# Performance work log

Hardware: AMD Instinct MI355X
Metric: run time of the kernel (lower is better)

Reference implementation:

```python
import jax, jax.numpy as jnp
import numpy as np

B, M, EMB, K = 32768, 2048, 128, 8
TAU = 0.3

def setup_inputs() -> dict:
    key = jax.random.key(0)
    ks = jax.random.split(key, 6)
    return {
        "Gl_cur": jax.random.normal(ks[0], (B, 2), dtype=jnp.float32),
        "ancL": jax.random.normal(ks[1], (B, M, 2), dtype=jnp.float32),
        "W1": jax.random.normal(ks[2], (EMB, 2), dtype=jnp.float32) * 0.5,
        "b1": jax.random.normal(ks[3], (EMB,), dtype=jnp.float32) * 0.1,
        "W2": jax.random.normal(ks[4], (EMB, EMB), dtype=jnp.float32) * (1.0 / np.sqrt(EMB)),
        "b2": jax.random.normal(ks[5], (EMB,), dtype=jnp.float32) * 0.1,
    }

def reference(Gl_cur, ancL, W1, b1, W2, b2):
    # pairwise squared distances: [B, M]
    d2 = jnp.sum((ancL - Gl_cur[:, None, :]) ** 2, axis=-1)
    # top-k nearest anchors (topk of -d2, as in torch code)
    vals, idxs = jax.lax.top_k(-d2, K)              # vals: [B,K] (negated d2)
    topA = jnp.take_along_axis(ancL, idxs[:, :, None], axis=1)  # [B,K,2]
    # 2-layer GELU MLP (exact/erf GELU, torch default); dropout inactive in eval
    h1 = jax.nn.gelu(jnp.einsum('bkc,ec->bke', topA, W1) + b1, approximate=False)
    topE = jax.nn.gelu(jnp.einsum('bke,fe->bkf', h1, W2) + b2, approximate=False)
    # softmax combine: w = softmax(vals / -tau) = softmax(d2_top / tau), faithful to source
    w = jax.nn.softmax(vals / (-TAU), axis=1)       # [B,K]
    return jnp.sum(topE * w[:, :, None], axis=1)    # [B, EMB]
```

## Files before the change

### kernel.cpp

```cpp
#include <hip/hip_runtime.h>
#include <hip/hip_bf16.h>
#include <math.h>

#define NB   32768
#define NM   2048
#define NEMB 128
#define NK   8
#define TAU  0.3f
#define FLT_BIG 3.402823466e38f

typedef __attribute__((ext_vector_type(8))) short bf16x8;
typedef __attribute__((ext_vector_type(4))) float f32x4;

__device__ __forceinline__ float gelu_tanh(float x) {
    const float x2 = x * x;
    const float u  = fmaf(0.044715f, x2, 1.0f);
    const float a  = x * u * (-2.3022082f);
    const float e  = __builtin_amdgcn_exp2f(a);
    const float r  = __builtin_amdgcn_rcpf(e + 1.0f);
    return x * r;
}
__device__ __forceinline__ unsigned pack2(float lo, float hi) {
    __hip_bfloat162 b = __float22bfloat162_rn(make_float2(lo, hi));
    return *reinterpret_cast<unsigned*>(&b);
}

template<int CTRL>
__device__ __forceinline__ unsigned dpp_umin(unsigned v) {
    const unsigned t = (unsigned)__builtin_amdgcn_update_dpp(0, (int)v, CTRL, 0xF, 0xF, true);
    return v < t ? v : t;
}
template<int CTRL>
__device__ __forceinline__ float dpp_fadd(float v) {
    const float t = __int_as_float(__builtin_amdgcn_update_dpp(0, __float_as_int(v), CTRL, 0xF, 0xF, true));
    return v + t;
}

template<int DEPTH>
__device__ __forceinline__ int extract8(float (&ld)[DEPTH], unsigned (&lp)[DEPTH],
                                        float (&td)[8], unsigned (&tp)[8], const int lane) {
    int pops = 0;
#pragma unroll
    for (int k = 0; k < 8; ++k) {
        const unsigned key = __float_as_uint(ld[0]);
        unsigned m = key;
        m = dpp_umin<0xB1>(m);  m = dpp_umin<0x4E>(m);
        m = dpp_umin<0x141>(m); m = dpp_umin<0x140>(m);
        { unsigned t = __shfl_xor(m, 16); m = m < t ? m : t;
          t = __shfl_xor(m, 32);          m = m < t ? m : t; }
        const unsigned long long mk = __ballot(key == m);
        const int src = __ffsll(mk) - 1;
        td[k] = __uint_as_float(m);
        tp[k] = __shfl(lp[0], src);
        if (lane == src) {
#pragma unroll
            for (int j = 0; j < DEPTH - 1; ++j) { ld[j] = ld[j + 1]; lp[j] = lp[j + 1]; }
            ld[DEPTH - 1] = FLT_BIG;
            ++pops;
        }
    }
    return pops;
}

__global__ void __launch_bounds__(512, 6) fused_anchor_mlp(
    const float* __restrict__ Gl, const float* __restrict__ ancL,
    const float* __restrict__ W1, const float* __restrict__ b1,
    const float* __restrict__ W2, const float* __restrict__ b2,
    float* __restrict__ out)
{
    __shared__ uint4  w2s[2048];
    __shared__ uint4  h1s4[1024];
    __shared__ float4 b2s4[32];
    __shared__ float  wts[8][8];

    const int tid  = threadIdx.x;
    const int wave = tid >> 6;
    const int lane = tid & 63;
    const int pair = wave >> 1;
    const int half = wave & 1;
    const int rowbase = blockIdx.x << 3;
    const int row  = rowbase + wave;

    {
        const float4* w2f = reinterpret_cast<const float4*>(W2);
        for (int i = tid; i < 2048; i += 512) {
            const float4 lo = w2f[i * 2], hi = w2f[i * 2 + 1];
            uint4 u;
            u.x = pack2(lo.x, lo.y); u.y = pack2(lo.z, lo.w);
            u.z = pack2(hi.x, hi.y); u.w = pack2(hi.z, hi.w);
            w2s[(i & ~15) | ((i & 15) ^ ((i >> 4) & 7))] = u;
        }
        if (tid < 32) b2s4[tid] = reinterpret_cast<const float4*>(b2)[tid];
    }

    const float2 g = reinterpret_cast<const float2*>(Gl)[row];
    const f32x4* a4 = reinterpret_cast<const f32x4*>(ancL) + (size_t)row * (NM / 2);

    float    bd[3];
    unsigned bp[3];
#pragma unroll
    for (int i = 0; i < 3; ++i) { bd[i] = FLT_BIG; bp[i] = 0u; }

    auto ins3 = [&](float d, unsigned p) {
        const bool c0 = d < bd[0], c1 = d < bd[1], c2 = d < bd[2];
        const float n2 = __builtin_amdgcn_fmed3f(d, bd[1], bd[2]);
        const float n1 = __builtin_amdgcn_fmed3f(d, bd[0], bd[1]);
        const float n0 = fminf(d, bd[0]);
        bp[2] = c1 ? bp[1] : (c2 ? p : bp[2]);
        bp[1] = c0 ? bp[0] : (c1 ? p : bp[1]);
        bp[0] = c0 ? p : bp[0];
        bd[2] = n2; bd[1] = n1; bd[0] = n0;
    };

    f32x4 buf[3];
#pragma unroll
    for (int j = 0; j < 3; ++j) buf[j] = __builtin_nontemporal_load(&a4[j * 64 + lane]);

#pragma unroll
    for (int it = 0; it < 16; ++it) {
        const int slot = it % 3;
        const f32x4 v = buf[slot];
        if (it + 3 < 16)
            buf[slot] = __builtin_nontemporal_load(&a4[(it + 3) * 64 + lane]);
        const float dx0 = v.x - g.x, dy0 = v.y - g.y;
        const float dx1 = v.z - g.x, dy1 = v.w - g.y;
        const float d0 = __fadd_rn(__fmul_rn(dx0, dx0), __fmul_rn(dy0, dy0));
        const float d1 = __fadd_rn(__fmul_rn(dx1, dx1), __fmul_rn(dy1, dy1));
        ins3(d0, pack2(v.x, v.y));
        ins3(d1, pack2(v.z, v.w));
    }

    float    td[8];
    unsigned tp[8];
    const int pops = extract8<3>(bd, bp, td, tp, lane);

    if (__ballot(pops == 3)) {
        float    fd[8];
        unsigned fp[8];
#pragma unroll
        for (int i = 0; i < 8; ++i) { fd[i] = FLT_BIG; fp[i] = 0u; }
        for (int it = 0; it < 16; ++it) {
            const f32x4 vv = a4[it * 64 + lane];
#pragma unroll
            for (int h = 0; h < 2; ++h) {
                const float ax = h ? vv.z : vv.x;
                const float ay = h ? vv.w : vv.y;
                const float ddx = ax - g.x, ddy = ay - g.y;
                const float d = __fadd_rn(__fmul_rn(ddx, ddx), __fmul_rn(ddy, ddy));
                if (d < fd[7]) {
                    const unsigned p = pack2(ax, ay);
#pragma unroll
                    for (int j = 7; j >= 1; --j) {
                        const bool s1 = fd[j - 1] > d;
                        const bool s2 = fd[j] > d;
                        const float    nd = s1 ? fd[j - 1] : (s2 ? d : fd[j]);
                        const unsigned np = s1 ? fp[j - 1] : (s2 ? p : fp[j]);
                        fd[j] = nd; fp[j] = np;
                    }
                    if (fd[0] > d) { fd[0] = d; fp[0] = p; }
                }
            }
        }
        (void)extract8<8>(fd, fp, td, tp, lane);
    }

    const float mx = td[7];
    float ek[8], ssum = 0.f;
#pragma unroll
    for (int k = 0; k < 8; ++k) { ek[k] = __expf((td[k] - mx) * (1.0f / TAU)); ssum += ek[k]; }
    const float inv = 1.0f / ssum;
    float wv = 0.f;
#pragma unroll
    for (int k = 0; k < 8; ++k) wv = (lane == k) ? ek[k] * inv : wv;
    if (lane < 8) wts[wave][lane] = wv;

    const float4 w1v = reinterpret_cast<const float4*>(W1)[lane];
    const float2 b1v = reinterpret_cast<const float2*>(b1)[lane];
    unsigned* h1w = reinterpret_cast<unsigned*>(h1s4 + (pair << 8));
#pragma unroll
    for (int k = 0; k < 8; ++k) {
        const unsigned pk = tp[k];
        const float ax = __uint_as_float(pk << 16);
        const float ay = __uint_as_float(pk & 0xFFFF0000u);
        const float x0 = fmaf(ax, w1v.x, fmaf(ay, w1v.y, b1v.x));
        const float x1 = fmaf(ax, w1v.z, fmaf(ay, w1v.w, b1v.y));
        const int r = (half << 3) + k;
        h1w[(r << 6) + ((((lane >> 2) ^ k) << 2) | (lane & 3))] = pack2(gelu_tanh(x0), gelu_tanh(x1));
    }
    __syncthreads();

    const uint4* h1b = h1s4 + (pair << 8);
    const int bslot = lane >> 4, bxor = lane & 7, brow = (lane & 15) * 16;
    bf16x8 bq0 = __builtin_bit_cast(bf16x8, h1b[brow + (( 0 + bslot) ^ bxor)]);
    bf16x8 bq1 = __builtin_bit_cast(bf16x8, h1b[brow + (( 4 + bslot) ^ bxor)]);
    bf16x8 bq2 = __builtin_bit_cast(bf16x8, h1b[brow + (( 8 + bslot) ^ bxor)]);
    bf16x8 bq3 = __builtin_bit_cast(bf16x8, h1b[brow + ((12 + bslot) ^ bxor)]);

    const float wsel = wts[(pair << 1) | ((lane >> 3) & 1)][lane & 7];

#pragma unroll 2
    for (int i = 0; i < 4; ++i) {
        const int ft = (half << 2) + i;
        const int arow = (ft * 16 + (lane & 15)) * 16;
        f32x4 acc = {0.f, 0.f, 0.f, 0.f};
        acc = __builtin_amdgcn_mfma_f32_16x16x32_bf16(
                  __builtin_bit_cast(bf16x8, w2s[arow + (( 0 + bslot) ^ bxor)]), bq0, acc, 0, 0, 0);
        acc = __builtin_amdgcn_mfma_f32_16x16x32_bf16(
                  __builtin_bit_cast(bf16x8, w2s[arow + (( 4 + bslot) ^ bxor)]), bq1, acc, 0, 0, 0);
        acc = __builtin_amdgcn_mfma_f32_16x16x32_bf16(
                  __builtin_bit_cast(bf16x8, w2s[arow + (( 8 + bslot) ^ bxor)]), bq2, acc, 0, 0, 0);
        acc = __builtin_amdgcn_mfma_f32_16x16x32_bf16(
                  __builtin_bit_cast(bf16x8, w2s[arow + ((12 + bslot) ^ bxor)]), bq3, acc, 0, 0, 0);

        const float4 b2v = b2s4[ft * 4 + (lane >> 4)];
        float s0 = gelu_tanh(acc[0] + b2v.x) * wsel;
        float s1 = gelu_tanh(acc[1] + b2v.y) * wsel;
        float s2 = gelu_tanh(acc[2] + b2v.z) * wsel;
        float s3 = gelu_tanh(acc[3] + b2v.w) * wsel;
        s0 = dpp_fadd<0xB1>(s0); s0 = dpp_fadd<0x4E>(s0); s0 = dpp_fadd<0x141>(s0);
        s1 = dpp_fadd<0xB1>(s1); s1 = dpp_fadd<0x4E>(s1); s1 = dpp_fadd<0x141>(s1);
        s2 = dpp_fadd<0xB1>(s2); s2 = dpp_fadd<0x4E>(s2); s2 = dpp_fadd<0x141>(s2);
        s3 = dpp_fadd<0xB1>(s3); s3 = dpp_fadd<0x4E>(s3); s3 = dpp_fadd<0x141>(s3);
        if ((lane & 7) == 0) {
            const int which = (lane >> 3) & 1;
            const size_t ob = (size_t)(rowbase + (pair << 1) + which) * NEMB
                              + ft * 16 + ((lane >> 4) << 2);
            *reinterpret_cast<float4*>(&out[ob]) = make_float4(s0, s1, s2, s3);
        }
    }
}

extern "C" void kernel_launch(void* const* d_in, const int* in_sizes, int n_in,
                              void* d_out, int out_size, void* d_ws, size_t ws_size,
                              hipStream_t stream)
{
    const float* Gl  = (const float*)d_in[0];
    const float* anc = (const float*)d_in[1];
    const float* W1  = (const float*)d_in[2];
    const float* b1  = (const float*)d_in[3];
    const float* W2  = (const float*)d_in[4];
    const float* b2  = (const float*)d_in[5];
    float* outp = (float*)d_out;

    fused_anchor_mlp<<<NB / 8, 512, 0, stream>>>(Gl, anc, W1, b1, W2, b2, outp);
}
```

Measured before the change: 133.3 us.

## Split fused kernel into separate KNN and MLP kernels via workspace

Splits the fused kernel into two. A 256-thread KNN kernel streams the anchors and writes the top-8 softmax weights and packed anchor coordinates to a workspace. A second kernel runs the bf16 MFMA MLP from that workspace. This frees the bandwidth-bound top-k scan from the large LDS footprint of the MLP stage, so more waves can be resident. It also changes the anchor loads from nontemporal to normal. The cost is an extra launch plus a small workspace write and read, and the workspace must be large enough.

```diff
diff --git a/kernel.cpp b/kernel.cpp
--- a/kernel.cpp
+++ b/kernel.cpp
@@ -62,36 +62,14 @@
     return pops;
 }
 
-__global__ void __launch_bounds__(512, 6) fused_anchor_mlp(
+__global__ void __launch_bounds__(256, 8) knn_phase1(
     const float* __restrict__ Gl, const float* __restrict__ ancL,
-    const float* __restrict__ W1, const float* __restrict__ b1,
-    const float* __restrict__ W2, const float* __restrict__ b2,
-    float* __restrict__ out)
+    uint2* __restrict__ ws2)
 {
-    __shared__ uint4  w2s[2048];
-    __shared__ uint4  h1s4[1024];
-    __shared__ float4 b2s4[32];
-    __shared__ float  wts[8][8];
-
     const int tid  = threadIdx.x;
     const int wave = tid >> 6;
     const int lane = tid & 63;
-    const int pair = wave >> 1;
-    const int half = wave & 1;
-    const int rowbase = blockIdx.x << 3;
-    const int row  = rowbase + wave;
-
-    {
-        const float4* w2f = reinterpret_cast<const float4*>(W2);
-        for (int i = tid; i < 2048; i += 512) {
-            const float4 lo = w2f[i * 2], hi = w2f[i * 2 + 1];
-            uint4 u;
-            u.x = pack2(lo.x, lo.y); u.y = pack2(lo.z, lo.w);
-            u.z = pack2(hi.x, hi.y); u.w = pack2(hi.z, hi.w);
-            w2s[(i & ~15) | ((i & 15) ^ ((i >> 4) & 7))] = u;
-        }
-        if (tid < 32) b2s4[tid] = reinterpret_cast<const float4*>(b2)[tid];
-    }
+    const int row  = (blockIdx.x << 2) + wave;
 
     const float2 g = reinterpret_cast<const float2*>(Gl)[row];
     const f32x4* a4 = reinterpret_cast<const f32x4*>(ancL) + (size_t)row * (NM / 2);
@@ -114,14 +92,13 @@
 
     f32x4 buf[3];
 #pragma unroll
-    for (int j = 0; j < 3; ++j) buf[j] = __builtin_nontemporal_load(&a4[j * 64 + lane]);
+    for (int j = 0; j < 3; ++j) buf[j] = a4[j * 64 + lane];
 
 #pragma unroll
     for (int it = 0; it < 16; ++it) {
         const int slot = it % 3;
         const f32x4 v = buf[slot];
-        if (it + 3 < 16)
-            buf[slot] = __builtin_nontemporal_load(&a4[(it + 3) * 64 + lane]);
+        if (it + 3 < 16) buf[slot] = a4[(it + 3) * 64 + lane];
         const float dx0 = v.x - g.x, dy0 = v.y - g.y;
         const float dx1 = v.z - g.x, dy1 = v.w - g.y;
         const float d0 = __fadd_rn(__fmul_rn(dx0, dx0), __fmul_rn(dy0, dy0));
@@ -169,17 +146,56 @@
 #pragma unroll
     for (int k = 0; k < 8; ++k) { ek[k] = __expf((td[k] - mx) * (1.0f / TAU)); ssum += ek[k]; }
     const float inv = 1.0f / ssum;
-    float wv = 0.f;
-#pragma unroll
-    for (int k = 0; k < 8; ++k) wv = (lane == k) ? ek[k] * inv : wv;
-    if (lane < 8) wts[wave][lane] = wv;
+    float    wv = 0.f;
+    unsigned pv = 0u;
+#pragma unroll
+    for (int k = 0; k < 8; ++k) {
+        wv = (lane == k) ? ek[k] * inv : wv;
+        pv = (lane == k) ? tp[k]       : pv;
+    }
+    if (lane < 8) ws2[(size_t)row * 8 + lane] = make_uint2(__float_as_uint(wv), pv);
+}
+
+__global__ void __launch_bounds__(512, 6) mlp_phase2(
+    const uint2* __restrict__ ws2,
+    const float* __restrict__ W1, const float* __restrict__ b1,
+    const float* __restrict__ W2, const float* __restrict__ b2,
+    float* __restrict__ out)
+{
+    __shared__ uint4  w2s[2048];
+    __shared__ uint4  h1s4[1024];
+    __shared__ float4 b2s4[32];
+    __shared__ float  wts[8][8];
+
+    const int tid  = threadIdx.x;
+    const int wave = tid >> 6;
+    const int lane = tid & 63;
+    const int pair = wave >> 1;
+    const int half = wave & 1;
+    const int rowbase = blockIdx.x << 3;
+    const int row  = rowbase + wave;
+
+    {
+        const float4* w2f = reinterpret_cast<const float4*>(W2);
+        for (int i = tid; i < 2048; i += 512) {
+            const float4 lo = w2f[i * 2], hi = w2f[i * 2 + 1];
+            uint4 u;
+            u.x = pack2(lo.x, lo.y); u.y = pack2(lo.z, lo.w);
+            u.z = pack2(hi.x, hi.y); u.w = pack2(hi.z, hi.w);
+            w2s[(i & ~15) | ((i & 15) ^ ((i >> 4) & 7))] = u;
+        }
+        if (tid < 32) b2s4[tid] = reinterpret_cast<const float4*>(b2)[tid];
+    }
+
+    const uint2 q = ws2[(size_t)row * 8 + (lane & 7)];
+    if (lane < 8) wts[wave][lane] = __uint_as_float(q.x);
 
     const float4 w1v = reinterpret_cast<const float4*>(W1)[lane];
     const float2 b1v = reinterpret_cast<const float2*>(b1)[lane];
     unsigned* h1w = reinterpret_cast<unsigned*>(h1s4 + (pair << 8));
 #pragma unroll
     for (int k = 0; k < 8; ++k) {
-        const unsigned pk = tp[k];
+        const unsigned pk = (unsigned)__shfl((int)q.y, k);
         const float ax = __uint_as_float(pk << 16);
         const float ay = __uint_as_float(pk & 0xFFFF0000u);
         const float x0 = fmaf(ax, w1v.x, fmaf(ay, w1v.y, b1v.x));
@@ -241,6 +257,8 @@
     const float* W2  = (const float*)d_in[4];
     const float* b2  = (const float*)d_in[5];
     float* outp = (float*)d_out;
-
-    fused_anchor_mlp<<<NB / 8, 512, 0, stream>>>(Gl, anc, W1, b1, W2, b2, outp);
-}
+    uint2* ws2  = (uint2*)d_ws;
+
+    knn_phase1<<<NB / 4, 256, 0, stream>>>(Gl, anc, ws2);
+    mlp_phase2<<<NB / 8, 512, 0, stream>>>(ws2, W1, b1, W2, b2, outp);
+}
```

Measured after the change: 154.8 us. 1.16x slower.
